# Optimization experiments

Hardware: AMD Instinct MI355X
Metric: run time of the kernel (lower is better)

## Reference

```python
import jax, jax.numpy as jnp
import numpy as np

Q_LATTICE = 4      # nested lattice alphabet size
QMAX_ACT = 127.0   # 2**(8-1) - 1 for 8-bit LSQ


def _lattice_quantize(x_blocks, G, Ginv, q):
    # x_blocks: [N, 8] rows are block vectors. Lattice point = z @ G, z integer.
    z = jnp.round(x_blocks @ Ginv)
    half = q // 2
    z_mod = jnp.mod(z + half, q) - half  # nested (mod-q) lattice, centered
    return z_mod @ G


def setup_inputs() -> dict:
    key = jax.random.key(0)
    k1, k2 = jax.random.split(key)
    O, I, BS = 4096, 4096, 8
    rng = np.random.default_rng(0)
    G_np = np.eye(BS, dtype=np.float64) + 0.1 * rng.standard_normal((BS, BS))
    Ginv_np = np.linalg.inv(G_np)
    return {
        "x": jax.random.normal(k1, (256, I), dtype=jnp.float32),
        "weight": jax.random.normal(k2, (O, I), dtype=jnp.float32),
        "bias": jnp.zeros((O,), dtype=jnp.float32),
        "theta_beta": jnp.ones((O, 1), dtype=jnp.float32),
        "alpha": jnp.ones((1,), dtype=jnp.float32),
        "G": jnp.asarray(G_np, dtype=jnp.float32),
        "Ginv": jnp.asarray(Ginv_np, dtype=jnp.float32),
    }


def reference(x, weight, bias, theta_beta, alpha, G, Ginv):
    O, I = weight.shape
    bs = G.shape[0]
    nblk = I // bs
    sg = jax.lax.stop_gradient

    # --- hierarchical nested-lattice weight quantization (row tiling) ---
    W_blocks = weight.reshape(O, nblk, bs)
    # theta_beta [O, k] -> mean over k -> [O, 1, 1], broadcast to all blocks
    scale_w = jnp.mean(theta_beta, axis=-1, keepdims=True)[:, None, :]
    W_scaled = (W_blocks * scale_w).reshape(-1, bs)
    # straight-through lattice quantize
    W_q = W_scaled + sg(_lattice_quantize(W_scaled, G, Ginv, Q_LATTICE) - W_scaled)
    W_q = W_q.reshape(O, I)

    # --- linear ---
    y = x @ W_q.T + bias

    # --- LSQ activation quantization ---
    a = jax.nn.relu(alpha) + 1e-8          # [1]
    y_clipped = y + sg(jnp.clip(y, -a, a) - y)  # ste_clip (clamp detached)
    s = a / QMAX_ACT
    y_scaled = y_clipped / s
    y_round = y_scaled + sg(jnp.round(y_scaled) - y_scaled)  # ste_round
    return y_round * s
```

## Files before the change

kernel.cpp:

```cpp
#include <hip/hip_runtime.h>

typedef __attribute__((ext_vector_type(8))) __bf16 bf16x8;
typedef __attribute__((ext_vector_type(4))) float f32x4;

#define M_ 256
#define N_ 4096
#define K_ 4096
#define SPLITK 4
#define KC (K_ / SPLITK)
#define BM 128
#define BN 128
#define BK 64
#define KSTEPS (KC / BK)
#define NCH 48
#define LDSBUF 49152



__device__ __forceinline__ unsigned short f2bf(float f) {
  unsigned int u = __builtin_bit_cast(unsigned int, f);
  u += 0x7fffu + ((u >> 16) & 1u);
  return (unsigned short)(u >> 16);
}

__device__ __forceinline__ void async16(const void* g, void* l) {
  __builtin_amdgcn_global_load_lds(
      (const __attribute__((address_space(1))) unsigned int*)g,
      (__attribute__((address_space(3))) unsigned int*)l, 16, 0, 0);
}

__device__ __forceinline__ float lsq1(float y, float a, float s) {
  float yc = fminf(fmaxf(y, -a), a);
  return rintf(yc / s) * s;
}


__global__ __launch_bounds__(256) void k_quant(const float* __restrict__ W,
                                               const float* __restrict__ theta,
                                               const float* __restrict__ Ginv,
                                               unsigned short* __restrict__ zq,
                                               int kTheta) {
  __shared__ float Gi[64];
  const int tid = threadIdx.x;
  if (tid < 64) Gi[tid] = Ginv[tid];
  __syncthreads();
  const int s = blockIdx.x * 256 + tid;
  const int lane6 = s & 63;
  const int tile = s >> 6;
  const int o  = ((tile >> 7) << 4) + (lane6 & 15);
  const int kb = ((tile & 127) << 2) + (lane6 >> 4);
  const float4* wp = (const float4*)(W + ((size_t)o << 12) + ((size_t)kb << 3));
  const float4 w0 = wp[0], w1 = wp[1];
  float sc = 0.f;
  for (int t = 0; t < kTheta; ++t) sc += theta[o * kTheta + t];
  sc /= (float)kTheta;
  const float wsv[8] = {w0.x * sc, w0.y * sc, w0.z * sc, w0.w * sc,
                        w1.x * sc, w1.y * sc, w1.z * sc, w1.w * sc};
  unsigned int packed[4] = {0u, 0u, 0u, 0u};
  const unsigned long long lut = 0x3F800000BF80C000ull;
#pragma unroll
  for (int i = 0; i < 8; ++i) {
    float t = 0.f;
#pragma unroll
    for (int j = 0; j < 8; ++j)
      t = __fadd_rn(t, __fmul_rn(wsv[j], Gi[j * 8 + i]));
    const int zi = (int)rintf(t);
    const int idx = (zi + 2) & 3;
    const unsigned int h = (unsigned int)((lut >> (idx * 16)) & 0xFFFFull);
    packed[i >> 1] |= h << ((i & 1) * 16);
  }
  *(uint4*)(zq + ((size_t)s << 3)) = make_uint4(packed[0], packed[1], packed[2], packed[3]);
}


__global__ __launch_bounds__(256) void k_xg(const float* __restrict__ x,
                                            const float* __restrict__ G,
                                            unsigned short* __restrict__ hi,
                                            unsigned short* __restrict__ lo) {
  __shared__ float Gs[64];
  const int tid = threadIdx.x;
  if (tid < 64) Gs[tid] = G[tid];
  __syncthreads();
  const int s = blockIdx.x * 256 + tid;
  const int lane6 = s & 63;
  const int tile = s >> 6;
  const int m  = ((tile >> 7) << 4) + (lane6 & 15);
  const int kb = ((tile & 127) << 2) + (lane6 >> 4);
  const float4* xp = (const float4*)(x + ((size_t)m << 12) + ((size_t)kb << 3));
  const float4 a0 = xp[0], a1 = xp[1];
  float xv[8] = {a0.x, a0.y, a0.z, a0.w, a1.x, a1.y, a1.z, a1.w};
  unsigned int ph[4] = {0u, 0u, 0u, 0u}, pl[4] = {0u, 0u, 0u, 0u};
#pragma unroll
  for (int i = 0; i < 8; ++i) {
    float t = 0.f;
#pragma unroll
    for (int j = 0; j < 8; ++j) t = fmaf(xv[j], Gs[i * 8 + j], t);
    const unsigned short hb = f2bf(t);
    const float hf = __builtin_bit_cast(float, (unsigned int)hb << 16);
    const unsigned short lb = f2bf(t - hf);
    ph[i >> 1] |= ((unsigned int)hb) << ((i & 1) * 16);
    pl[i >> 1] |= ((unsigned int)lb) << ((i & 1) * 16);
  }
  *(uint4*)(hi + ((size_t)s << 3)) = make_uint4(ph[0], ph[1], ph[2], ph[3]);
  *(uint4*)(lo + ((size_t)s << 3)) = make_uint4(pl[0], pl[1], pl[2], pl[3]);
}


__global__ __launch_bounds__(512, 2) void k_gemm(const unsigned short* __restrict__ xgh,
                                                 const unsigned short* __restrict__ xgl,
                                                 const unsigned short* __restrict__ z,
                                                 float* __restrict__ part) {
  __shared__ uint4 smem4[2 * LDSBUF / 16];
  char* smem = (char*)smem4;

  const int tid = threadIdx.x;
  const int lane = tid & 63, wave = tid >> 6;
  const int wr = wave >> 1, wc = wave & 1;
  const int b = blockIdx.x;
  const int mt = b & 1;
  const int sk = (b >> 1) & 3;
  const int nt = b >> 3;
  const int k0t = sk * (KC / 32);
  const int rowa16 = mt * (BM / 16);
  const int rowb16 = nt * (BN / 16);
  const int lrow = lane & 15, lkg = lane >> 4;

  const unsigned short* src[6];
  unsigned int ldso[6];
#pragma unroll
  for (int ci = 0; ci < 6; ++ci) {
    const int c = wave * 6 + ci;
    const unsigned short* P;
    int rt;
    if (c < 16)      { P = xgh; rt = rowa16 + (c >> 1); }
    else if (c < 32) { P = xgl; rt = rowa16 + ((c - 16) >> 1); }
    else             { P = z;   rt = rowb16 + ((c - 32) >> 1); }
    src[ci] = P + (((size_t)(rt * 128 + k0t + (c & 1))) << 9) + lane * 8;
    ldso[ci] = (unsigned int)c * 1024u;
  }

  f32x4 acc[2][4] = {};

#pragma unroll
  for (int ci = 0; ci < 6; ++ci) async16(src[ci], smem + ldso[ci]);
  __syncthreads();

  for (int ks = 0; ks < KSTEPS; ++ks) {
    const int cur = (ks & 1) * LDSBUF;
    const int nxt = LDSBUF - cur;
    if (ks + 1 < KSTEPS) {
#pragma unroll
      for (int ci = 0; ci < 6; ++ci)
        async16(src[ci] + (size_t)(ks + 1) * 1024, smem + nxt + ldso[ci]);
    }

#pragma unroll
    for (int kk = 0; kk < 2; ++kk) {
      bf16x8 bfr[4], ah[2], al[2];
#pragma unroll
      for (int nf = 0; nf < 4; ++nf)
        bfr[nf] = *(const bf16x8*)(smem + cur + (32 + (wc * 4 + nf) * 2 + kk) * 1024 + lane * 16);
#pragma unroll
      for (int mf = 0; mf < 2; ++mf) {
        ah[mf] = *(const bf16x8*)(smem + cur + ((wr * 2 + mf) * 2 + kk) * 1024 + lane * 16);
        al[mf] = *(const bf16x8*)(smem + cur + (16 + (wr * 2 + mf) * 2 + kk) * 1024 + lane * 16);
      }
#pragma unroll
      for (int mf = 0; mf < 2; ++mf)
#pragma unroll
        for (int nf = 0; nf < 4; ++nf) {
          acc[mf][nf] = __builtin_amdgcn_mfma_f32_16x16x32_bf16(ah[mf], bfr[nf], acc[mf][nf], 0, 0, 0);
          acc[mf][nf] = __builtin_amdgcn_mfma_f32_16x16x32_bf16(al[mf], bfr[nf], acc[mf][nf], 0, 0, 0);
        }
    }
    __syncthreads();
  }

  float* pb = part + (size_t)sk * (M_ * N_);
  const int row_a = mt * BM, row_b = nt * BN;
#pragma unroll
  for (int mf = 0; mf < 2; ++mf)
#pragma unroll
    for (int nf = 0; nf < 4; ++nf)
#pragma unroll
      for (int r = 0; r < 4; ++r) {
        const int m = row_a + wr * 32 + mf * 16 + lkg * 4 + r;
        const int n = row_b + wc * 64 + nf * 16 + lrow;
        pb[(size_t)m * N_ + n] = acc[mf][nf][r];
      }
}


__global__ __launch_bounds__(256) void k_epi(const float* __restrict__ part,
                                             const float* __restrict__ bias,
                                             const float* __restrict__ alpha,
                                             float* __restrict__ out) {
  const int i4 = blockIdx.x * 256 + threadIdx.x;
  const size_t off = (size_t)i4 * 4;
  const float4 p0 = *(const float4*)(part + off);
  const float4 p1 = *(const float4*)(part + (size_t)1 * M_ * N_ + off);
  const float4 p2 = *(const float4*)(part + (size_t)2 * M_ * N_ + off);
  const float4 p3 = *(const float4*)(part + (size_t)3 * M_ * N_ + off);
  const int n = (int)(off & (N_ - 1));
  const float4 bv = *(const float4*)(bias + n);
  const float a = fmaxf(alpha[0], 0.f) + 1e-8f;
  const float s = a / 127.0f;
  float4 o;
  o.x = lsq1(((p0.x + p1.x) + p2.x) + p3.x + bv.x, a, s);
  o.y = lsq1(((p0.y + p1.y) + p2.y) + p3.y + bv.y, a, s);
  o.z = lsq1(((p0.z + p1.z) + p2.z) + p3.z + bv.z, a, s);
  o.w = lsq1(((p0.w + p1.w) + p2.w) + p3.w + bv.w, a, s);
  *(float4*)(out + off) = o;
}


extern "C" void kernel_launch(void* const* d_in, const int* in_sizes, int n_in,
                              void* d_out, int out_size, void* d_ws, size_t ws_size,
                              hipStream_t stream) {
  const float* x     = (const float*)d_in[0];
  const float* W     = (const float*)d_in[1];
  const float* bias  = (const float*)d_in[2];
  const float* theta = (const float*)d_in[3];
  const float* alpha = (const float*)d_in[4];
  const float* G     = (const float*)d_in[5];
  const float* Ginv  = (const float*)d_in[6];
  float* out = (float*)d_out;

  const int O = in_sizes[2];
  const int kTheta = in_sizes[3] / O;

  char* ws = (char*)d_ws;
  unsigned short* zq  = (unsigned short*)ws;
  unsigned short* xgh = (unsigned short*)(ws + 33554432);
  unsigned short* xgl = (unsigned short*)(ws + 35651584);
  float* part = (float*)(ws + 37748736);
  if (ws_size < 54525952) return;

  k_quant<<<(N_ * K_ / 8) / 256, 256, 0, stream>>>(W, theta, Ginv, zq, kTheta);
  k_xg<<<(M_ * K_ / 8) / 256, 256, 0, stream>>>(x, G, xgh, xgl);
  k_gemm<<<2 * 4 * 32, 512, 0, stream>>>(xgh, xgl, zq, part);
  k_epi<<<(M_ * N_ / 4) / 256, 256, 0, stream>>>(part, bias, alpha, out);
}
```

Before: 52.07 us.

## Fuse prep kernels and shrink GEMM tiles to BN=64, BK=32 for more blocks

The weight-quantization and x@G preprocessing kernels are merged into one launch that branches on block index, which removes a kernel launch. The GEMM tile shrinks from 128x128x64 to 128x64x32, doubling the grid to 512 blocks. LDS use drops, so launch bounds now allow 4 blocks per CU, giving better occupancy and more even load across CUs. In exchange, each block reuses less data per tile and synchronizes more often, since there are twice as many K steps with half the MFMA work per barrier.

```diff
diff --git a/kernel.cpp b/kernel.cpp
--- a/kernel.cpp
+++ b/kernel.cpp
@@ -9,11 +9,11 @@
 #define SPLITK 4
 #define KC (K_ / SPLITK)
 #define BM 128
-#define BN 128
-#define BK 64
+#define BN 64
+#define BK 32
 #define KSTEPS (KC / BK)
-#define NCH 48
-#define LDSBUF 49152
+#define NCH 20
+#define LDSBUF 20480
 
 
 
@@ -35,78 +35,79 @@
 }
 
 
-__global__ __launch_bounds__(256) void k_quant(const float* __restrict__ W,
-                                               const float* __restrict__ theta,
-                                               const float* __restrict__ Ginv,
-                                               unsigned short* __restrict__ zq,
-                                               int kTheta) {
-  __shared__ float Gi[64];
+#define NQB ((N_ * K_ / 8) / 256)
+#define NXB ((M_ * K_ / 8) / 256)
+
+__global__ __launch_bounds__(256) void k_prep(const float* __restrict__ W,
+                                              const float* __restrict__ theta,
+                                              const float* __restrict__ Ginv,
+                                              const float* __restrict__ x,
+                                              const float* __restrict__ G,
+                                              unsigned short* __restrict__ zq,
+                                              unsigned short* __restrict__ hi,
+                                              unsigned short* __restrict__ lo,
+                                              int kTheta) {
+  __shared__ float Ms[64];
   const int tid = threadIdx.x;
-  if (tid < 64) Gi[tid] = Ginv[tid];
+  const bool isQ = blockIdx.x < NQB;
+  if (tid < 64) Ms[tid] = isQ ? Ginv[tid] : G[tid];
   __syncthreads();
-  const int s = blockIdx.x * 256 + tid;
-  const int lane6 = s & 63;
-  const int tile = s >> 6;
-  const int o  = ((tile >> 7) << 4) + (lane6 & 15);
-  const int kb = ((tile & 127) << 2) + (lane6 >> 4);
-  const float4* wp = (const float4*)(W + ((size_t)o << 12) + ((size_t)kb << 3));
-  const float4 w0 = wp[0], w1 = wp[1];
-  float sc = 0.f;
-  for (int t = 0; t < kTheta; ++t) sc += theta[o * kTheta + t];
-  sc /= (float)kTheta;
-  const float wsv[8] = {w0.x * sc, w0.y * sc, w0.z * sc, w0.w * sc,
-                        w1.x * sc, w1.y * sc, w1.z * sc, w1.w * sc};
-  unsigned int packed[4] = {0u, 0u, 0u, 0u};
-  const unsigned long long lut = 0x3F800000BF80C000ull;
-#pragma unroll
-  for (int i = 0; i < 8; ++i) {
-    float t = 0.f;
-#pragma unroll
-    for (int j = 0; j < 8; ++j)
-      t = __fadd_rn(t, __fmul_rn(wsv[j], Gi[j * 8 + i]));
-    const int zi = (int)rintf(t);
-    const int idx = (zi + 2) & 3;
-    const unsigned int h = (unsigned int)((lut >> (idx * 16)) & 0xFFFFull);
-    packed[i >> 1] |= h << ((i & 1) * 16);
+
+  if (isQ) {
+    const int s = blockIdx.x * 256 + tid;
+    const int lane6 = s & 63;
+    const int tile = s >> 6;
+    const int o  = ((tile >> 7) << 4) + (lane6 & 15);
+    const int kb = ((tile & 127) << 2) + (lane6 >> 4);
+    const float4* wp = (const float4*)(W + ((size_t)o << 12) + ((size_t)kb << 3));
+    const float4 w0 = wp[0], w1 = wp[1];
+    float sc = 0.f;
+    for (int t = 0; t < kTheta; ++t) sc += theta[o * kTheta + t];
+    sc /= (float)kTheta;
+    const float wsv[8] = {w0.x * sc, w0.y * sc, w0.z * sc, w0.w * sc,
+                          w1.x * sc, w1.y * sc, w1.z * sc, w1.w * sc};
+    unsigned int packed[4] = {0u, 0u, 0u, 0u};
+    const unsigned long long lut = 0x3F800000BF80C000ull;
+#pragma unroll
+    for (int i = 0; i < 8; ++i) {
+      float t = 0.f;
+#pragma unroll
+      for (int j = 0; j < 8; ++j)
+        t = __fadd_rn(t, __fmul_rn(wsv[j], Ms[j * 8 + i]));
+      const int zi = (int)rintf(t);
+      const int idx = (zi + 2) & 3;
+      const unsigned int h = (unsigned int)((lut >> (idx * 16)) & 0xFFFFull);
+      packed[i >> 1] |= h << ((i & 1) * 16);
+    }
+    *(uint4*)(zq + ((size_t)s << 3)) = make_uint4(packed[0], packed[1], packed[2], packed[3]);
+  } else {
+    const int s = (blockIdx.x - NQB) * 256 + tid;
+    const int lane6 = s & 63;
+    const int tile = s >> 6;
+    const int m  = ((tile >> 7) << 4) + (lane6 & 15);
+    const int kb = ((tile & 127) << 2) + (lane6 >> 4);
+    const float4* xp = (const float4*)(x + ((size_t)m << 12) + ((size_t)kb << 3));
+    const float4 a0 = xp[0], a1 = xp[1];
+    float xv[8] = {a0.x, a0.y, a0.z, a0.w, a1.x, a1.y, a1.z, a1.w};
+    unsigned int ph[4] = {0u, 0u, 0u, 0u}, pl[4] = {0u, 0u, 0u, 0u};
+#pragma unroll
+    for (int i = 0; i < 8; ++i) {
+      float t = 0.f;
+#pragma unroll
+      for (int j = 0; j < 8; ++j) t = fmaf(xv[j], Ms[i * 8 + j], t);
+      const unsigned short hb = f2bf(t);
+      const float hf = __builtin_bit_cast(float, (unsigned int)hb << 16);
+      const unsigned short lb = f2bf(t - hf);
+      ph[i >> 1] |= ((unsigned int)hb) << ((i & 1) * 16);
+      pl[i >> 1] |= ((unsigned int)lb) << ((i & 1) * 16);
+    }
+    *(uint4*)(hi + ((size_t)s << 3)) = make_uint4(ph[0], ph[1], ph[2], ph[3]);
+    *(uint4*)(lo + ((size_t)s << 3)) = make_uint4(pl[0], pl[1], pl[2], pl[3]);
   }
-  *(uint4*)(zq + ((size_t)s << 3)) = make_uint4(packed[0], packed[1], packed[2], packed[3]);
-}
-
-
-__global__ __launch_bounds__(256) void k_xg(const float* __restrict__ x,
-                                            const float* __restrict__ G,
-                                            unsigned short* __restrict__ hi,
-                                            unsigned short* __restrict__ lo) {
-  __shared__ float Gs[64];
-  const int tid = threadIdx.x;
-  if (tid < 64) Gs[tid] = G[tid];
-  __syncthreads();
-  const int s = blockIdx.x * 256 + tid;
-  const int lane6 = s & 63;
-  const int tile = s >> 6;
-  const int m  = ((tile >> 7) << 4) + (lane6 & 15);
-  const int kb = ((tile & 127) << 2) + (lane6 >> 4);
-  const float4* xp = (const float4*)(x + ((size_t)m << 12) + ((size_t)kb << 3));
-  const float4 a0 = xp[0], a1 = xp[1];
-  float xv[8] = {a0.x, a0.y, a0.z, a0.w, a1.x, a1.y, a1.z, a1.w};
-  unsigned int ph[4] = {0u, 0u, 0u, 0u}, pl[4] = {0u, 0u, 0u, 0u};
-#pragma unroll
-  for (int i = 0; i < 8; ++i) {
-    float t = 0.f;
-#pragma unroll
-    for (int j = 0; j < 8; ++j) t = fmaf(xv[j], Gs[i * 8 + j], t);
-    const unsigned short hb = f2bf(t);
-    const float hf = __builtin_bit_cast(float, (unsigned int)hb << 16);
-    const unsigned short lb = f2bf(t - hf);
-    ph[i >> 1] |= ((unsigned int)hb) << ((i & 1) * 16);
-    pl[i >> 1] |= ((unsigned int)lb) << ((i & 1) * 16);
-  }
-  *(uint4*)(hi + ((size_t)s << 3)) = make_uint4(ph[0], ph[1], ph[2], ph[3]);
-  *(uint4*)(lo + ((size_t)s << 3)) = make_uint4(pl[0], pl[1], pl[2], pl[3]);
-}
-
-
-__global__ __launch_bounds__(512, 2) void k_gemm(const unsigned short* __restrict__ xgh,
+}
+
+
+__global__ __launch_bounds__(512, 4) void k_gemm(const unsigned short* __restrict__ xgh,
                                                  const unsigned short* __restrict__ xgl,
                                                  const unsigned short* __restrict__ z,
                                                  float* __restrict__ part) {
@@ -125,54 +126,55 @@
   const int rowb16 = nt * (BN / 16);
   const int lrow = lane & 15, lkg = lane >> 4;
 
-  const unsigned short* src[6];
-  unsigned int ldso[6];
-#pragma unroll
-  for (int ci = 0; ci < 6; ++ci) {
-    const int c = wave * 6 + ci;
-    const unsigned short* P;
-    int rt;
-    if (c < 16)      { P = xgh; rt = rowa16 + (c >> 1); }
-    else if (c < 32) { P = xgl; rt = rowa16 + ((c - 16) >> 1); }
-    else             { P = z;   rt = rowb16 + ((c - 32) >> 1); }
-    src[ci] = P + (((size_t)(rt * 128 + k0t + (c & 1))) << 9) + lane * 8;
-    ldso[ci] = (unsigned int)c * 1024u;
+  const unsigned short* src[3];
+  unsigned int ldso[3];
+#pragma unroll
+  for (int ci = 0; ci < 3; ++ci) {
+    const int c = ci * 8 + wave;
+    if (c < NCH) {
+      const unsigned short* P;
+      int rt;
+      if (c < 8)       { P = xgh; rt = rowa16 + c; }
+      else if (c < 16) { P = xgl; rt = rowa16 + (c - 8); }
+      else             { P = z;   rt = rowb16 + (c - 16); }
+      src[ci] = P + (((size_t)(rt * 128 + k0t)) << 9) + lane * 8;
+      ldso[ci] = (unsigned int)c * 1024u;
+    } else {
+      src[ci] = nullptr;
+      ldso[ci] = 0;
+    }
   }
-
-  f32x4 acc[2][4] = {};
-
-#pragma unroll
-  for (int ci = 0; ci < 6; ++ci) async16(src[ci], smem + ldso[ci]);
+  const int nchunk = (wave < 4) ? 3 : 2;
+
+  f32x4 acc[2][2] = {};
+
+  for (int ci = 0; ci < nchunk; ++ci) async16(src[ci], smem + ldso[ci]);
   __syncthreads();
 
   for (int ks = 0; ks < KSTEPS; ++ks) {
     const int cur = (ks & 1) * LDSBUF;
     const int nxt = LDSBUF - cur;
     if (ks + 1 < KSTEPS) {
-#pragma unroll
-      for (int ci = 0; ci < 6; ++ci)
-        async16(src[ci] + (size_t)(ks + 1) * 1024, smem + nxt + ldso[ci]);
-    }
-
-#pragma unroll
-    for (int kk = 0; kk < 2; ++kk) {
-      bf16x8 bfr[4], ah[2], al[2];
-#pragma unroll
-      for (int nf = 0; nf < 4; ++nf)
-        bfr[nf] = *(const bf16x8*)(smem + cur + (32 + (wc * 4 + nf) * 2 + kk) * 1024 + lane * 16);
-#pragma unroll
-      for (int mf = 0; mf < 2; ++mf) {
-        ah[mf] = *(const bf16x8*)(smem + cur + ((wr * 2 + mf) * 2 + kk) * 1024 + lane * 16);
-        al[mf] = *(const bf16x8*)(smem + cur + (16 + (wr * 2 + mf) * 2 + kk) * 1024 + lane * 16);
+      for (int ci = 0; ci < nchunk; ++ci)
+        async16(src[ci] + (size_t)(ks + 1) * 512, smem + nxt + ldso[ci]);
+    }
+
+    bf16x8 bfr[2], ah[2], al[2];
+#pragma unroll
+    for (int nf = 0; nf < 2; ++nf)
+      bfr[nf] = *(const bf16x8*)(smem + cur + (16 + wc * 2 + nf) * 1024 + lane * 16);
+#pragma unroll
+    for (int mf = 0; mf < 2; ++mf) {
+      ah[mf] = *(const bf16x8*)(smem + cur + (wr * 2 + mf) * 1024 + lane * 16);
+      al[mf] = *(const bf16x8*)(smem + cur + (8 + wr * 2 + mf) * 1024 + lane * 16);
+    }
+#pragma unroll
+    for (int mf = 0; mf < 2; ++mf)
+#pragma unroll
+      for (int nf = 0; nf < 2; ++nf) {
+        acc[mf][nf] = __builtin_amdgcn_mfma_f32_16x16x32_bf16(ah[mf], bfr[nf], acc[mf][nf], 0, 0, 0);
+        acc[mf][nf] = __builtin_amdgcn_mfma_f32_16x16x32_bf16(al[mf], bfr[nf], acc[mf][nf], 0, 0, 0);
       }
-#pragma unroll
-      for (int mf = 0; mf < 2; ++mf)
-#pragma unroll
-        for (int nf = 0; nf < 4; ++nf) {
-          acc[mf][nf] = __builtin_amdgcn_mfma_f32_16x16x32_bf16(ah[mf], bfr[nf], acc[mf][nf], 0, 0, 0);
-          acc[mf][nf] = __builtin_amdgcn_mfma_f32_16x16x32_bf16(al[mf], bfr[nf], acc[mf][nf], 0, 0, 0);
-        }
-    }
     __syncthreads();
   }
 
@@ -181,11 +183,11 @@
 #pragma unroll
   for (int mf = 0; mf < 2; ++mf)
 #pragma unroll
-    for (int nf = 0; nf < 4; ++nf)
+    for (int nf = 0; nf < 2; ++nf)
 #pragma unroll
       for (int r = 0; r < 4; ++r) {
         const int m = row_a + wr * 32 + mf * 16 + lkg * 4 + r;
-        const int n = row_b + wc * 64 + nf * 16 + lrow;
+        const int n = row_b + wc * 32 + nf * 16 + lrow;
         pb[(size_t)m * N_ + n] = acc[mf][nf][r];
       }
 }
@@ -236,8 +238,7 @@
   float* part = (float*)(ws + 37748736);
   if (ws_size < 54525952) return;
 
-  k_quant<<<(N_ * K_ / 8) / 256, 256, 0, stream>>>(W, theta, Ginv, zq, kTheta);
-  k_xg<<<(M_ * K_ / 8) / 256, 256, 0, stream>>>(x, G, xgh, xgl);
-  k_gemm<<<2 * 4 * 32, 512, 0, stream>>>(xgh, xgl, zq, part);
+  k_prep<<<NQB + NXB, 256, 0, stream>>>(W, theta, Ginv, x, G, zq, xgh, xgl, kTheta);
+  k_gemm<<<2 * 4 * 64, 512, 0, stream>>>(xgh, xgl, zq, part);
   k_epi<<<(M_ * N_ / 4) / 256, 256, 0, stream>>>(part, bias, alpha, out);
 }
```

After: 52.40 us. No clear change (+0.6%).
